# Kernel optimization log

Hardware: AMD Instinct MI355X
Metric: run time of the kernel (lower is better)

The kernel has to match this reference:

```python
import jax, jax.numpy as jnp
import numpy as np

N = 50000        # nodes
E = 800000       # edges (avg degree 16)
F_IN = 256       # cfg.dataset.features
H = 256          # cfg.model.hidden_size


def setup_inputs() -> dict:
    key = jax.random.key(0)
    ks = jax.random.split(key, 8)
    x = jax.random.normal(ks[0], (N, F_IN), dtype=jnp.float32)
    edge_index = jax.random.randint(ks[1], (2, E), 0, N, dtype=jnp.int32)
    # GCNConv weights: layer0 in->hidden, layer1 hidden->hidden, layer2 hidden->1
    W0 = jax.random.normal(ks[2], (F_IN, H), jnp.float32) / np.sqrt(F_IN)
    b0 = jnp.zeros((H,), jnp.float32)
    W1 = jax.random.normal(ks[3], (H, H), jnp.float32) / np.sqrt(H)
    b1 = jnp.zeros((H,), jnp.float32)
    W2 = jax.random.normal(ks[4], (H, 1), jnp.float32) / np.sqrt(H)
    b2 = jnp.zeros((1,), jnp.float32)
    return {"x": x, "edge_index": edge_index, "W0": W0, "b0": b0,
            "W1": W1, "b1": b1, "W2": W2, "b2": b2}


def reference(x, edge_index, W0, b0, W1, b1, W2, b2):
    n = x.shape[0]
    loop = jnp.arange(n, dtype=edge_index.dtype)
    # gcn_norm with self-loops: Ahat = D^{-1/2} (A + I) D^{-1/2}
    src = jnp.concatenate([edge_index[0], loop])  # [E+N]
    dst = jnp.concatenate([edge_index[1], loop])  # [E+N]
    deg = jax.ops.segment_sum(jnp.ones_like(src, dtype=x.dtype), dst, num_segments=n)
    dinv = jnp.where(deg > 0, jax.lax.rsqrt(deg), 0.0)
    norm = dinv[src] * dinv[dst]                  # [E+N]

    def gcn_layer(h, W, b):
        h = h @ W                                              # [N, out]
        agg = jax.ops.segment_sum(norm[:, None] * h[src], dst, num_segments=n)
        return agg + b

    h = jax.nn.relu(gcn_layer(x, W0, b0))
    h = jax.nn.relu(gcn_layer(h, W1, b1))
    return gcn_layer(h, W2, b2)                                # [N, 1]
```

## Files before the change

kernel.cpp:

```cpp
#include <hip/hip_runtime.h>


static inline size_t alignup(size_t x, size_t a) { return (x + a - 1) & ~(a - 1); }

typedef __attribute__((ext_vector_type(8))) short short8;
typedef __attribute__((ext_vector_type(4))) float f32x4;

__device__ inline unsigned short f2bf(float f) {
    union { float f; unsigned int u; } v; v.f = f;
    unsigned int r = v.u + 0x7FFFu + ((v.u >> 16) & 1u);
    return (unsigned short)(r >> 16);
}
__device__ inline float bf2f(unsigned short u) {
    union { unsigned int u; float f; } v; v.u = ((unsigned int)u) << 16;
    return v.f;
}

__global__ __launch_bounds__(256) void k_fill_i32(int* __restrict__ p, int v, int n) {
    int i = blockIdx.x * 256 + threadIdx.x;
    if (i < n) p[i] = v;
}

__global__ __launch_bounds__(256) void k_count_deg(const int* __restrict__ dst, int* __restrict__ deg, int E) {
    int e = blockIdx.x * 256 + threadIdx.x;
    if (e < E) atomicAdd(&deg[dst[e]], 1);
}

__global__ __launch_bounds__(256) void k_dinv(const int* __restrict__ deg, float* __restrict__ dinv, int n) {
    int i = blockIdx.x * 256 + threadIdx.x;
    if (i < n) dinv[i] = rsqrtf((float)deg[i] + 1.0f);
}

__global__ __launch_bounds__(256) void k_scan1(const int* __restrict__ deg, int* __restrict__ rs,
                                               int* __restrict__ bsum, int n) {
    __shared__ int sd[256];
    int b = blockIdx.x, tid = threadIdx.x;
    int base = b * 1024 + tid * 4;
    int v[4];
#pragma unroll
    for (int j = 0; j < 4; ++j) v[j] = (base + j < n) ? deg[base + j] : 0;
    int tot = v[0] + v[1] + v[2] + v[3];
    sd[tid] = tot;
    for (int off = 1; off < 256; off <<= 1) {
        __syncthreads();
        int t = (tid >= off) ? sd[tid - off] : 0;
        __syncthreads();
        sd[tid] += t;
    }
    __syncthreads();
    int run = tid ? sd[tid - 1] : 0;
#pragma unroll
    for (int j = 0; j < 4; ++j) {
        if (base + j < n) rs[base + j] = run;
        run += v[j];
    }
    if (tid == 255) bsum[b] = sd[255];
}

__global__ __launch_bounds__(256) void k_scan2(int* __restrict__ bsum, int nb) {
    __shared__ int sd[256];
    int tid = threadIdx.x;
    sd[tid] = (tid < nb) ? bsum[tid] : 0;
    for (int off = 1; off < 256; off <<= 1) {
        __syncthreads();
        int t = (tid >= off) ? sd[tid - off] : 0;
        __syncthreads();
        sd[tid] += t;
    }
    __syncthreads();
    if (tid < nb) bsum[tid] = tid ? sd[tid - 1] : 0;
}

__global__ __launch_bounds__(256) void k_scan3(int* __restrict__ rs, int* __restrict__ cursor,
                                               const int* __restrict__ bsum, int n, int E) {
    int b = blockIdx.x, tid = threadIdx.x;
    int off = bsum[b];
    int base = b * 1024 + tid * 4;
#pragma unroll
    for (int j = 0; j < 4; ++j) {
        int idx = base + j;
        if (idx < n) {
            int v = rs[idx] + off;
            rs[idx] = v;
            cursor[idx] = v;
        }
    }
    if (b == 0 && tid == 0) rs[n] = E;
}

__global__ __launch_bounds__(256) void k_fill_csr(const int* __restrict__ src, const int* __restrict__ dst,
                                                  int* __restrict__ cursor, int* __restrict__ col, int E) {
    int e = blockIdx.x * 256 + threadIdx.x;
    if (e < E) {
        int d = dst[e];
        int pos = atomicAdd(&cursor[d], 1);
        col[pos] = src[e];
    }
}

__global__ __launch_bounds__(256) void k_wt(const float* __restrict__ W, unsigned short* __restrict__ Wt) {
    int idx = blockIdx.x * 256 + threadIdx.x;
    int k = idx >> 8, n = idx & 255;
    Wt[(size_t)n * 256 + k] = f2bf(W[(size_t)k * 256 + n]);
}

__global__ __launch_bounds__(256) void k_gemm_mfma(const float* __restrict__ A,
                                                   const unsigned short* __restrict__ Wt,
                                                   unsigned short* __restrict__ C,
                                                   const float* __restrict__ dinv, int N) {
    __shared__ __align__(16) unsigned short As2[128 * 32];
    __shared__ __align__(16) unsigned short Bs2[128 * 32];
    __shared__ __align__(16) unsigned short Cs[4 * 64 * 64];

    int tid = threadIdx.x;
    int lane = tid & 63, w = tid >> 6;
    int wr = w >> 1, wc = w & 1;
    int row0 = blockIdx.y * 128, col0 = blockIdx.x * 128;

    f32x4 acc[4][4];
#pragma unroll
    for (int m = 0; m < 4; ++m)
#pragma unroll
        for (int n = 0; n < 4; ++n) acc[m][n] = (f32x4)0.f;

    for (int k0 = 0; k0 < 256; k0 += 32) {
#pragma unroll
        for (int it = 0; it < 2; ++it) {
            int c = tid + it * 256;
            int r = c >> 2, kg = c & 3;
            int grow = row0 + r;
            float4 f0 = make_float4(0.f, 0.f, 0.f, 0.f), f1 = f0;
            if (grow < N) {
                const float* g = A + (size_t)grow * 256 + k0 + kg * 8;
                f0 = *(const float4*)g;
                f1 = *(const float4*)(g + 4);
            }
            short8 u;
            u[0] = (short)f2bf(f0.x); u[1] = (short)f2bf(f0.y);
            u[2] = (short)f2bf(f0.z); u[3] = (short)f2bf(f0.w);
            u[4] = (short)f2bf(f1.x); u[5] = (short)f2bf(f1.y);
            u[6] = (short)f2bf(f1.z); u[7] = (short)f2bf(f1.w);
            *(short8*)&As2[(r >> 4) * 512 + kg * 128 + (r & 15) * 8] = u;
        }
#pragma unroll
        for (int it = 0; it < 2; ++it) {
            int c = tid + it * 256;
            int n = c >> 2, kg = c & 3;
            short8 u = *(const short8*)(Wt + (size_t)(col0 + n) * 256 + k0 + kg * 8);
            *(short8*)&Bs2[(n >> 4) * 512 + kg * 128 + (n & 15) * 8] = u;
        }
        __syncthreads();
        short8 af[4], bfr[4];
#pragma unroll
        for (int m = 0; m < 4; ++m)
            af[m] = *(const short8*)&As2[(wr * 4 + m) * 512 + (lane >> 4) * 128 + (lane & 15) * 8];
#pragma unroll
        for (int n = 0; n < 4; ++n)
            bfr[n] = *(const short8*)&Bs2[(wc * 4 + n) * 512 + (lane >> 4) * 128 + (lane & 15) * 8];
#pragma unroll
        for (int m = 0; m < 4; ++m)
#pragma unroll
            for (int n = 0; n < 4; ++n)
                acc[m][n] = __builtin_amdgcn_mfma_f32_16x16x32_bf16(af[m], bfr[n], acc[m][n], 0, 0, 0);
        __syncthreads();
    }

    unsigned short* myCs = &Cs[w * 4096];
#pragma unroll
    for (int m = 0; m < 4; ++m) {
#pragma unroll
        for (int j = 0; j < 4; ++j) {
            int r = m * 16 + (lane >> 4) * 4 + j;
            int grow = row0 + wr * 64 + r;
            float d = (grow < N) ? dinv[grow] : 0.f;
#pragma unroll
            for (int n = 0; n < 4; ++n)
                myCs[r * 64 + n * 16 + (lane & 15)] = f2bf(acc[m][n][j] * d);
        }
    }
    __syncthreads();
#pragma unroll
    for (int i = 0; i < 8; ++i) {
        int r = i * 8 + (lane >> 3);
        int grow = row0 + wr * 64 + r;
        if (grow < N) {
            short8 v = *(const short8*)&myCs[r * 64 + (lane & 7) * 8];
            *(short8*)(C + (size_t)grow * 256 + col0 + wc * 64 + (lane & 7) * 8) = v;
        }
    }
}

__global__ __launch_bounds__(256) void k_agg(const unsigned short* __restrict__ t, float* __restrict__ h,
                                             const int* __restrict__ rs, const int* __restrict__ col,
                                             const float* __restrict__ dinv, const float* __restrict__ bias,
                                             int N, int do_relu) {
    int wid = (blockIdx.x * 256 + threadIdx.x) >> 6;
    int lane = threadIdx.x & 63;
    if (wid >= N) return;
    const ushort4* tp = (const ushort4*)t;

    ushort4 sv = tp[(size_t)wid * 64 + lane];
    float a0 = bf2f(sv.x), a1 = bf2f(sv.y), a2 = bf2f(sv.z), a3 = bf2f(sv.w);

    int e0 = rs[wid], e1 = rs[wid + 1];
    for (int base = e0; base < e1; base += 64) {
        int m = e1 - base; if (m > 64) m = 64;
        int c = (base + lane < e1) ? col[base + lane] : 0;
        int j = 0;
        for (; j + 4 <= m; j += 4) {
            int s0 = __shfl(c, j), s1 = __shfl(c, j + 1), s2 = __shfl(c, j + 2), s3 = __shfl(c, j + 3);
            ushort4 v0 = tp[(size_t)s0 * 64 + lane];
            ushort4 v1 = tp[(size_t)s1 * 64 + lane];
            ushort4 v2 = tp[(size_t)s2 * 64 + lane];
            ushort4 v3 = tp[(size_t)s3 * 64 + lane];
            a0 += (bf2f(v0.x) + bf2f(v1.x)) + (bf2f(v2.x) + bf2f(v3.x));
            a1 += (bf2f(v0.y) + bf2f(v1.y)) + (bf2f(v2.y) + bf2f(v3.y));
            a2 += (bf2f(v0.z) + bf2f(v1.z)) + (bf2f(v2.z) + bf2f(v3.z));
            a3 += (bf2f(v0.w) + bf2f(v1.w)) + (bf2f(v2.w) + bf2f(v3.w));
        }
        for (; j < m; ++j) {
            int s = __shfl(c, j);
            ushort4 v = tp[(size_t)s * 64 + lane];
            a0 += bf2f(v.x); a1 += bf2f(v.y); a2 += bf2f(v.z); a3 += bf2f(v.w);
        }
    }
    float d = dinv[wid];
    float4 bv = ((const float4*)bias)[lane];
    float4 o = make_float4(fmaf(d, a0, bv.x), fmaf(d, a1, bv.y), fmaf(d, a2, bv.z), fmaf(d, a3, bv.w));
    if (do_relu) {
        o.x = fmaxf(o.x, 0.f); o.y = fmaxf(o.y, 0.f);
        o.z = fmaxf(o.z, 0.f); o.w = fmaxf(o.w, 0.f);
    }
    ((float4*)(h + (size_t)wid * 256))[lane] = o;
}

__global__ __launch_bounds__(256) void k_gemv(const float* __restrict__ h, const float* __restrict__ w,
                                              const float* __restrict__ dinv, float* __restrict__ z, int N) {
    int wid = (blockIdx.x * 256 + threadIdx.x) >> 6;
    int lane = threadIdx.x & 63;
    if (wid >= N) return;
    float4 hv = ((const float4*)(h + (size_t)wid * 256))[lane];
    float4 wv = ((const float4*)w)[lane];
    float s = hv.x * wv.x + hv.y * wv.y + hv.z * wv.z + hv.w * wv.w;
#pragma unroll
    for (int off = 32; off > 0; off >>= 1) s += __shfl_down(s, off, 64);
    if (lane == 0) z[wid] = dinv[wid] * s;
}

__global__ __launch_bounds__(256) void k_agg_out(const float* __restrict__ z, float* __restrict__ out,
                                                 const int* __restrict__ rs, const int* __restrict__ col,
                                                 const float* __restrict__ dinv, const float* __restrict__ b2,
                                                 int N) {
    int wid = (blockIdx.x * 256 + threadIdx.x) >> 6;
    int lane = threadIdx.x & 63;
    if (wid >= N) return;
    int e0 = rs[wid], e1 = rs[wid + 1];
    float v = 0.f;
    for (int base = e0; base < e1; base += 64) {
        int e = base + lane;
        if (e < e1) v += z[col[e]];
    }
#pragma unroll
    for (int off = 32; off > 0; off >>= 1) v += __shfl_down(v, off, 64);
    if (lane == 0) out[wid] = fmaf(dinv[wid], v + z[wid], b2[0]);
}

extern "C" void kernel_launch(void* const* d_in, const int* in_sizes, int n_in,
                              void* d_out, int out_size, void* d_ws, size_t ws_size,
                              hipStream_t stream) {
    const float* x  = (const float*)d_in[0];
    const int*   ei = (const int*)d_in[1];
    const float* W0 = (const float*)d_in[2];
    const float* b0 = (const float*)d_in[3];
    const float* W1 = (const float*)d_in[4];
    const float* b1 = (const float*)d_in[5];
    const float* W2 = (const float*)d_in[6];
    const float* b2 = (const float*)d_in[7];
    float* out = (float*)d_out;

    int N = in_sizes[0] / 256;
    int E = in_sizes[1] / 2;
    const int* esrc = ei;
    const int* edst = ei + E;

    char* p = (char*)d_ws;
    unsigned short* tb = (unsigned short*)p; p += alignup((size_t)N * 256 * 2, 16);
    float* h = (float*)p;      p += (size_t)N * 256 * 4;
    unsigned short* Wt0 = (unsigned short*)p; p += 256 * 256 * 2;
    unsigned short* Wt1 = (unsigned short*)p; p += 256 * 256 * 2;
    float* z = (float*)p;      p += alignup((size_t)N * 4, 16);
    float* dinv = (float*)p;   p += alignup((size_t)N * 4, 16);
    int* deg = (int*)p;        p += alignup((size_t)N * 4, 16);
    int* cursor = (int*)p;     p += alignup((size_t)N * 4, 16);
    int* rs = (int*)p;         p += alignup((size_t)(N + 1) * 4, 16);
    int* col = (int*)p;        p += alignup((size_t)E * 4, 16);
    int* bsum = (int*)p;       p += 256 * 4;

    int nb = (N + 1023) / 1024;
    dim3 blk(256);

    k_fill_i32<<<(N + 255) / 256, blk, 0, stream>>>(deg, 0, N);
    k_count_deg<<<(E + 255) / 256, blk, 0, stream>>>(edst, deg, E);
    k_dinv<<<(N + 255) / 256, blk, 0, stream>>>(deg, dinv, N);
    k_scan1<<<nb, blk, 0, stream>>>(deg, rs, bsum, N);
    k_scan2<<<1, blk, 0, stream>>>(bsum, nb);
    k_scan3<<<nb, blk, 0, stream>>>(rs, cursor, bsum, N, E);
    k_fill_csr<<<(E + 255) / 256, blk, 0, stream>>>(esrc, edst, cursor, col, E);
    k_wt<<<256, blk, 0, stream>>>(W0, Wt0);
    k_wt<<<256, blk, 0, stream>>>(W1, Wt1);

    dim3 gg(2, (N + 127) / 128);
    k_gemm_mfma<<<gg, blk, 0, stream>>>(x, Wt0, tb, dinv, N);
    k_agg<<<(N + 3) / 4, blk, 0, stream>>>(tb, h, rs, col, dinv, b0, N, 1);
    k_gemm_mfma<<<gg, blk, 0, stream>>>(h, Wt1, tb, dinv, N);
    k_agg<<<(N + 3) / 4, blk, 0, stream>>>(tb, h, rs, col, dinv, b1, N, 1);
    k_gemv<<<(N + 3) / 4, blk, 0, stream>>>(h, W2, dinv, z, N);
    k_agg_out<<<(N + 3) / 4, blk, 0, stream>>>(z, out, rs, col, dinv, b2, N);
}
```

Before: 394.7 us.

## Store hidden activations in bf16, pre-convert x, and widen aggregation loads

Hidden activations h are now stored as bf16 instead of fp32, which halves the write traffic of the aggregation and the read traffic of the second GEMM and the GEMV. x is converted to bf16 once in a separate kernel, so the GEMM loads bf16 directly. The aggregation kernel now has each half-wave gather a different neighbour row with 16-byte loads, then combines the two halves with a shuffle. Smaller changes fold the dinv computation into the scan and merge the two weight-transpose launches. The extra x conversion pass costs one read and write of x, and rounding h to bf16 adds some precision loss.

New measurement: 384.8 us. 2.5% less time.

```diff
diff --git a/kernel.cpp b/kernel.cpp
--- a/kernel.cpp
+++ b/kernel.cpp
@@ -26,13 +26,8 @@
     if (e < E) atomicAdd(&deg[dst[e]], 1);
 }
 
-__global__ __launch_bounds__(256) void k_dinv(const int* __restrict__ deg, float* __restrict__ dinv, int n) {
-    int i = blockIdx.x * 256 + threadIdx.x;
-    if (i < n) dinv[i] = rsqrtf((float)deg[i] + 1.0f);
-}
-
 __global__ __launch_bounds__(256) void k_scan1(const int* __restrict__ deg, int* __restrict__ rs,
-                                               int* __restrict__ bsum, int n) {
+                                               int* __restrict__ bsum, float* __restrict__ dinv, int n) {
     __shared__ int sd[256];
     int b = blockIdx.x, tid = threadIdx.x;
     int base = b * 1024 + tid * 4;
@@ -51,7 +46,10 @@
     int run = tid ? sd[tid - 1] : 0;
 #pragma unroll
     for (int j = 0; j < 4; ++j) {
-        if (base + j < n) rs[base + j] = run;
+        if (base + j < n) {
+            rs[base + j] = run;
+            dinv[base + j] = rsqrtf((float)v[j] + 1.0f);
+        }
         run += v[j];
     }
     if (tid == 255) bsum[b] = sd[255];
@@ -98,13 +96,31 @@
     }
 }
 
-__global__ __launch_bounds__(256) void k_wt(const float* __restrict__ W, unsigned short* __restrict__ Wt) {
+__global__ __launch_bounds__(256) void k_wt2(const float* __restrict__ W0, const float* __restrict__ W1,
+                                             unsigned short* __restrict__ Wt0, unsigned short* __restrict__ Wt1) {
     int idx = blockIdx.x * 256 + threadIdx.x;
-    int k = idx >> 8, n = idx & 255;
+    const float* W = (idx < 65536) ? W0 : W1;
+    unsigned short* Wt = (idx < 65536) ? Wt0 : Wt1;
+    int id = idx & 65535;
+    int k = id >> 8, n = id & 255;
     Wt[(size_t)n * 256 + k] = f2bf(W[(size_t)k * 256 + n]);
 }
 
-__global__ __launch_bounds__(256) void k_gemm_mfma(const float* __restrict__ A,
+__global__ __launch_bounds__(256) void k_xb(const float* __restrict__ x, unsigned short* __restrict__ xb,
+                                            int total8) {
+    int i = blockIdx.x * 256 + threadIdx.x;
+    if (i >= total8) return;
+    float4 f0 = *(const float4*)(x + (size_t)i * 8);
+    float4 f1 = *(const float4*)(x + (size_t)i * 8 + 4);
+    short8 u;
+    u[0] = (short)f2bf(f0.x); u[1] = (short)f2bf(f0.y);
+    u[2] = (short)f2bf(f0.z); u[3] = (short)f2bf(f0.w);
+    u[4] = (short)f2bf(f1.x); u[5] = (short)f2bf(f1.y);
+    u[6] = (short)f2bf(f1.z); u[7] = (short)f2bf(f1.w);
+    *(short8*)(xb + (size_t)i * 8) = u;
+}
+
+__global__ __launch_bounds__(256) void k_gemm_mfma(const unsigned short* __restrict__ A,
                                                    const unsigned short* __restrict__ Wt,
                                                    unsigned short* __restrict__ C,
                                                    const float* __restrict__ dinv, int N) {
@@ -129,17 +145,8 @@
             int c = tid + it * 256;
             int r = c >> 2, kg = c & 3;
             int grow = row0 + r;
-            float4 f0 = make_float4(0.f, 0.f, 0.f, 0.f), f1 = f0;
-            if (grow < N) {
-                const float* g = A + (size_t)grow * 256 + k0 + kg * 8;
-                f0 = *(const float4*)g;
-                f1 = *(const float4*)(g + 4);
-            }
-            short8 u;
-            u[0] = (short)f2bf(f0.x); u[1] = (short)f2bf(f0.y);
-            u[2] = (short)f2bf(f0.z); u[3] = (short)f2bf(f0.w);
-            u[4] = (short)f2bf(f1.x); u[5] = (short)f2bf(f1.y);
-            u[6] = (short)f2bf(f1.z); u[7] = (short)f2bf(f1.w);
+            short8 u = {0, 0, 0, 0, 0, 0, 0, 0};
+            if (grow < N) u = *(const short8*)(A + (size_t)grow * 256 + k0 + kg * 8);
             *(short8*)&As2[(r >> 4) * 512 + kg * 128 + (r & 15) * 8] = u;
         }
 #pragma unroll
@@ -190,58 +197,85 @@
     }
 }
 
-__global__ __launch_bounds__(256) void k_agg(const unsigned short* __restrict__ t, float* __restrict__ h,
+__global__ __launch_bounds__(256) void k_agg(const unsigned short* __restrict__ t,
+                                             unsigned short* __restrict__ h,
                                              const int* __restrict__ rs, const int* __restrict__ col,
                                              const float* __restrict__ dinv, const float* __restrict__ bias,
                                              int N, int do_relu) {
     int wid = (blockIdx.x * 256 + threadIdx.x) >> 6;
     int lane = threadIdx.x & 63;
     if (wid >= N) return;
-    const ushort4* tp = (const ushort4*)t;
-
-    ushort4 sv = tp[(size_t)wid * 64 + lane];
-    float a0 = bf2f(sv.x), a1 = bf2f(sv.y), a2 = bf2f(sv.z), a3 = bf2f(sv.w);
+    int half = lane >> 5, sub = lane & 31;
+    const short8* tp = (const short8*)t;
+
+    short8 sv = tp[(size_t)wid * 32 + sub];
+    float hsel = (half == 0) ? 1.f : 0.f;
+    float a[8];
+#pragma unroll
+    for (int i = 0; i < 8; ++i) a[i] = hsel * bf2f((unsigned short)sv[i]);
 
     int e0 = rs[wid], e1 = rs[wid + 1];
     for (int base = e0; base < e1; base += 64) {
         int m = e1 - base; if (m > 64) m = 64;
         int c = (base + lane < e1) ? col[base + lane] : 0;
+        int npairs = (m + 1) >> 1;
         int j = 0;
-        for (; j + 4 <= m; j += 4) {
-            int s0 = __shfl(c, j), s1 = __shfl(c, j + 1), s2 = __shfl(c, j + 2), s3 = __shfl(c, j + 3);
-            ushort4 v0 = tp[(size_t)s0 * 64 + lane];
-            ushort4 v1 = tp[(size_t)s1 * 64 + lane];
-            ushort4 v2 = tp[(size_t)s2 * 64 + lane];
-            ushort4 v3 = tp[(size_t)s3 * 64 + lane];
-            a0 += (bf2f(v0.x) + bf2f(v1.x)) + (bf2f(v2.x) + bf2f(v3.x));
-            a1 += (bf2f(v0.y) + bf2f(v1.y)) + (bf2f(v2.y) + bf2f(v3.y));
-            a2 += (bf2f(v0.z) + bf2f(v1.z)) + (bf2f(v2.z) + bf2f(v3.z));
-            a3 += (bf2f(v0.w) + bf2f(v1.w)) + (bf2f(v2.w) + bf2f(v3.w));
-        }
-        for (; j < m; ++j) {
-            int s = __shfl(c, j);
-            ushort4 v = tp[(size_t)s * 64 + lane];
-            a0 += bf2f(v.x); a1 += bf2f(v.y); a2 += bf2f(v.z); a3 += bf2f(v.w);
-        }
-    }
-    float d = dinv[wid];
-    float4 bv = ((const float4*)bias)[lane];
-    float4 o = make_float4(fmaf(d, a0, bv.x), fmaf(d, a1, bv.y), fmaf(d, a2, bv.z), fmaf(d, a3, bv.w));
-    if (do_relu) {
-        o.x = fmaxf(o.x, 0.f); o.y = fmaxf(o.y, 0.f);
-        o.z = fmaxf(o.z, 0.f); o.w = fmaxf(o.w, 0.f);
-    }
-    ((float4*)(h + (size_t)wid * 256))[lane] = o;
-}
-
-__global__ __launch_bounds__(256) void k_gemv(const float* __restrict__ h, const float* __restrict__ w,
+        for (; j + 4 <= npairs; j += 4) {
+            int i0 = 2 * j + half, i1 = i0 + 2, i2 = i0 + 4, i3 = i0 + 6;
+            int s0 = __shfl(c, i0), s1 = __shfl(c, i1), s2 = __shfl(c, i2), s3 = __shfl(c, i3);
+            float f0 = (i0 < m) ? 1.f : 0.f, f1 = (i1 < m) ? 1.f : 0.f;
+            float f2 = (i2 < m) ? 1.f : 0.f, f3 = (i3 < m) ? 1.f : 0.f;
+            short8 w0 = tp[(size_t)s0 * 32 + sub];
+            short8 w1 = tp[(size_t)s1 * 32 + sub];
+            short8 w2 = tp[(size_t)s2 * 32 + sub];
+            short8 w3 = tp[(size_t)s3 * 32 + sub];
+#pragma unroll
+            for (int i = 0; i < 8; ++i) {
+                a[i] = fmaf(f0, bf2f((unsigned short)w0[i]), a[i]);
+                a[i] = fmaf(f1, bf2f((unsigned short)w1[i]), a[i]);
+                a[i] = fmaf(f2, bf2f((unsigned short)w2[i]), a[i]);
+                a[i] = fmaf(f3, bf2f((unsigned short)w3[i]), a[i]);
+            }
+        }
+        for (; j < npairs; ++j) {
+            int i0 = 2 * j + half;
+            int s0 = __shfl(c, i0);
+            float f0 = (i0 < m) ? 1.f : 0.f;
+            short8 w0 = tp[(size_t)s0 * 32 + sub];
+#pragma unroll
+            for (int i = 0; i < 8; ++i) a[i] = fmaf(f0, bf2f((unsigned short)w0[i]), a[i]);
+        }
+    }
+#pragma unroll
+    for (int i = 0; i < 8; ++i) a[i] += __shfl_xor(a[i], 32, 64);
+
+    if (half == 0) {
+        float d = dinv[wid];
+        float4 b0 = ((const float4*)bias)[sub * 2];
+        float4 b1 = ((const float4*)bias)[sub * 2 + 1];
+        float o[8];
+        o[0] = fmaf(d, a[0], b0.x); o[1] = fmaf(d, a[1], b0.y);
+        o[2] = fmaf(d, a[2], b0.z); o[3] = fmaf(d, a[3], b0.w);
+        o[4] = fmaf(d, a[4], b1.x); o[5] = fmaf(d, a[5], b1.y);
+        o[6] = fmaf(d, a[6], b1.z); o[7] = fmaf(d, a[7], b1.w);
+        short8 u;
+#pragma unroll
+        for (int i = 0; i < 8; ++i) {
+            float v = do_relu ? fmaxf(o[i], 0.f) : o[i];
+            u[i] = (short)f2bf(v);
+        }
+        *(short8*)(h + (size_t)wid * 256 + sub * 8) = u;
+    }
+}
+
+__global__ __launch_bounds__(256) void k_gemv(const unsigned short* __restrict__ h, const float* __restrict__ w,
                                               const float* __restrict__ dinv, float* __restrict__ z, int N) {
     int wid = (blockIdx.x * 256 + threadIdx.x) >> 6;
     int lane = threadIdx.x & 63;
     if (wid >= N) return;
-    float4 hv = ((const float4*)(h + (size_t)wid * 256))[lane];
+    ushort4 hv = ((const ushort4*)(h + (size_t)wid * 256))[lane];
     float4 wv = ((const float4*)w)[lane];
-    float s = hv.x * wv.x + hv.y * wv.y + hv.z * wv.z + hv.w * wv.w;
+    float s = bf2f(hv.x) * wv.x + bf2f(hv.y) * wv.y + bf2f(hv.z) * wv.z + bf2f(hv.w) * wv.w;
 #pragma unroll
     for (int off = 32; off > 0; off >>= 1) s += __shfl_down(s, off, 64);
     if (lane == 0) z[wid] = dinv[wid] * s;
@@ -285,7 +319,8 @@
 
     char* p = (char*)d_ws;
     unsigned short* tb = (unsigned short*)p; p += alignup((size_t)N * 256 * 2, 16);
-    float* h = (float*)p;      p += (size_t)N * 256 * 4;
+    unsigned short* hb = (unsigned short*)p; p += alignup((size_t)N * 256 * 2, 16);
+    unsigned short* xb = (unsigned short*)p; p += alignup((size_t)N * 256 * 2, 16);
     unsigned short* Wt0 = (unsigned short*)p; p += 256 * 256 * 2;
     unsigned short* Wt1 = (unsigned short*)p; p += 256 * 256 * 2;
     float* z = (float*)p;      p += alignup((size_t)N * 4, 16);
@@ -301,19 +336,19 @@
 
     k_fill_i32<<<(N + 255) / 256, blk, 0, stream>>>(deg, 0, N);
     k_count_deg<<<(E + 255) / 256, blk, 0, stream>>>(edst, deg, E);
-    k_dinv<<<(N + 255) / 256, blk, 0, stream>>>(deg, dinv, N);
-    k_scan1<<<nb, blk, 0, stream>>>(deg, rs, bsum, N);
+    k_scan1<<<nb, blk, 0, stream>>>(deg, rs, bsum, dinv, N);
     k_scan2<<<1, blk, 0, stream>>>(bsum, nb);
     k_scan3<<<nb, blk, 0, stream>>>(rs, cursor, bsum, N, E);
     k_fill_csr<<<(E + 255) / 256, blk, 0, stream>>>(esrc, edst, cursor, col, E);
-    k_wt<<<256, blk, 0, stream>>>(W0, Wt0);
-    k_wt<<<256, blk, 0, stream>>>(W1, Wt1);
+    k_wt2<<<512, blk, 0, stream>>>(W0, W1, Wt0, Wt1);
+    int total8 = N * 32;
+    k_xb<<<(total8 + 255) / 256, blk, 0, stream>>>(x, xb, total8);
 
     dim3 gg(2, (N + 127) / 128);
-    k_gemm_mfma<<<gg, blk, 0, stream>>>(x, Wt0, tb, dinv, N);
-    k_agg<<<(N + 3) / 4, blk, 0, stream>>>(tb, h, rs, col, dinv, b0, N, 1);
-    k_gemm_mfma<<<gg, blk, 0, stream>>>(h, Wt1, tb, dinv, N);
-    k_agg<<<(N + 3) / 4, blk, 0, stream>>>(tb, h, rs, col, dinv, b1, N, 1);
-    k_gemv<<<(N + 3) / 4, blk, 0, stream>>>(h, W2, dinv, z, N);
+    k_gemm_mfma<<<gg, blk, 0, stream>>>(xb, Wt0, tb, dinv, N);
+    k_agg<<<(N + 3) / 4, blk, 0, stream>>>(tb, hb, rs, col, dinv, b0, N, 1);
+    k_gemm_mfma<<<gg, blk, 0, stream>>>(hb, Wt1, tb, dinv, N);
+    k_agg<<<(N + 3) / 4, blk, 0, stream>>>(tb, hb, rs, col, dinv, b1, N, 1);
+    k_gemv<<<(N + 3) / 4, blk, 0, stream>>>(hb, W2, dinv, z, N);
     k_agg_out<<<(N + 3) / 4, blk, 0, stream>>>(z, out, rs, col, dinv, b2, N);
 }
```
